# Performance work log

Measured on AMD Instinct MI355X. Metric: run time of the kernel, lower is better.

Reference implementation:

```python
import jax, jax.numpy as jnp
import numpy as np

T = 32          # timesteps
GAIN = 1.0      # input_gain
TAU = 2.0       # LIF membrane time constant
VTH = 1.0       # v_threshold
VRESET = 0.0    # v_reset (hard reset)
ALPHA = 2.0     # ATan surrogate alpha


@jax.custom_vjp
def heaviside_atan(x):
    # forward: Heaviside spike; backward: ATan surrogate gradient
    return (x >= 0).astype(x.dtype)

def _hs_fwd(x):
    return heaviside_atan(x), x

def _hs_bwd(x, g):
    # d/dx ATan surrogate: (alpha/2) / (1 + (pi/2 * alpha * x)^2)
    return (g * (ALPHA / 2.0) / (1.0 + (jnp.pi / 2.0 * ALPHA * x) ** 2),)

heaviside_atan.defvjp(_hs_fwd, _hs_bwd)


def lif_multistep(cur_seq):
    """Multi-step LIF over cur_seq [T, B, H]; hard reset, detach_reset=True."""
    def step(v, x):
        # charge: v = v + (x - (v - v_reset)) / tau
        v = v + (x - (v - VRESET)) / TAU
        spike = heaviside_atan(v - VTH)
        sd = jax.lax.stop_gradient(spike)  # detach_reset
        v = (1.0 - sd) * v + sd * VRESET   # hard reset
        return v, spike

    v0 = jnp.full(cur_seq.shape[1:], VRESET, dtype=cur_seq.dtype)
    _, spikes = jax.lax.scan(step, v0, cur_seq)
    return spikes


def setup_inputs() -> dict:
    key = jax.random.key(0)
    ks = jax.random.split(key, 4)

    def xavier(k, o, i):
        lim = np.sqrt(6.0 / (i + o)).astype(np.float32)
        return jax.random.uniform(k, (o, i), minval=-lim, maxval=lim, dtype=jnp.float32)

    x_flat = jax.random.uniform(ks[0], (512, 784), dtype=jnp.float32)
    W0 = xavier(ks[1], 1024, 784)
    b0 = jnp.zeros((1024,), jnp.float32)
    W1 = xavier(ks[2], 1024, 1024)
    b1 = jnp.zeros((1024,), jnp.float32)
    W2 = xavier(ks[3], 10, 1024)
    b2 = jnp.zeros((10,), jnp.float32)
    return {"x_flat": x_flat, "W0": W0, "b0": b0, "W1": W1, "b1": b1, "W2": W2, "b2": b2}


def reference(x_flat, W0, b0, W1, b1, W2, b2):
    # repeat_static_input: [B, 784] -> [T, B, 784]
    h = jnp.broadcast_to(x_flat * GAIN, (T,) + x_flat.shape)
    count = None
    for W, b in ((W0, b0), (W1, b1), (W2, b2)):
        cur = jnp.einsum('tbi,oi->tbo', h, W) + b  # fc over all timesteps
        spk = lif_multistep(cur)                   # [T, B, out]
        count = spk.sum(axis=0)                    # spike counts [B, out]
        h = spk
    # predict() returns argmax(count); return the final count (logits) here
    return count
```

## Files before the change

kernel.cpp:

```cpp
#include <hip/hip_runtime.h>
#include <hip/hip_bf16.h>
#include <stdint.h>


typedef __bf16 bf16x8 __attribute__((ext_vector_type(8)));
typedef float  f32x4  __attribute__((ext_vector_type(4)));

__device__ __forceinline__ void gload16(const void* g, void* l) {
  __builtin_amdgcn_global_load_lds((const __attribute__((address_space(1))) void*)g,
                                   (__attribute__((address_space(3))) void*)l,
                                   16, 0, 0);
}

__device__ __forceinline__ void bsplit3(float v, __hip_bfloat16& h,
                                        __hip_bfloat16& m, __hip_bfloat16& l) {
  h = __float2bfloat16(v);
  float r1 = v - __bfloat162float(h);
  m = __float2bfloat16(r1);
  float r2 = r1 - __bfloat162float(m);
  l = __float2bfloat16(r2);
}

__global__ __launch_bounds__(256) void prep_k(const float* __restrict__ x,
                                              const float* __restrict__ W0,
                                              __hip_bfloat16* __restrict__ Ax,
                                              __hip_bfloat16* __restrict__ Bw) {
  const int bid = blockIdx.x, tid = threadIdx.x;
  if (bid < 1600) {
    int i = bid * 256 + tid;
    int m = i / 800, k = i - m * 800;
    float v = (k < 784) ? x[(size_t)m * 784 + k] : 0.f;
    __hip_bfloat16 h, mm, l;
    bsplit3(v, h, mm, l);
    size_t base = (size_t)m * 4800;
    Ax[base + k] = h;         Ax[base + 800 + k] = h;
    Ax[base + 1600 + k] = mm; Ax[base + 2400 + k] = mm;
    Ax[base + 3200 + k] = h;  Ax[base + 4000 + k] = l;
  } else {
    int i = (bid - 1600) * 256 + tid;
    int n = i / 800, k = i - n * 800;
    float v = (k < 784) ? W0[(size_t)n * 784 + k] : 0.f;
    __hip_bfloat16 h, mm, l;
    bsplit3(v, h, mm, l);
    size_t base = (size_t)n * 4800;
    Bw[base + k] = h;         Bw[base + 800 + k] = mm;
    Bw[base + 1600 + k] = h;  Bw[base + 2400 + k] = mm;
    Bw[base + 3200 + k] = l;  Bw[base + 4000 + k] = h;
  }
}

__global__ __launch_bounds__(256, 2) void gemm0t_k(const __hip_bfloat16* __restrict__ A,
                                                   const __hip_bfloat16* __restrict__ B,
                                                   const float* __restrict__ W1,
                                                   float* __restrict__ W1T,
                                                   float* __restrict__ Cpart) {
  __shared__ __align__(16) char smem[16384];
  const int bid = blockIdx.x, tid = threadIdx.x;

  if (bid >= 320) {
    float (*t)[33] = (float(*)[33])smem;
    int tt = bid - 320;
    int c0 = (tt & 31) * 32, r0 = (tt >> 5) * 32;
    int lx = tid & 31, ly = tid >> 5;
#pragma unroll
    for (int i = 0; i < 32; i += 8)
      t[ly + i][lx] = W1[(size_t)(r0 + ly + i) * 1024 + (c0 + lx)];
    __syncthreads();
#pragma unroll
    for (int i = 0; i < 32; i += 8)
      W1T[(size_t)(c0 + ly + i) * 1024 + (r0 + lx)] = t[lx][ly + i];
    return;
  }

  __hip_bfloat16* As = (__hip_bfloat16*)smem;
  __hip_bfloat16* Bs = As + 128 * 32;
  const int bx = bid & 3, by = (bid >> 2) & 7, bz = bid >> 5;
  const int wave = tid >> 6, lane = tid & 63, quad = lane >> 4, l16 = lane & 15;
  const int wm = (wave >> 1) * 64, wn = (wave & 1) * 64;
  const int mbase = bx * 128, nbase = by * 128, kbase = bz * 480;
  const int srow = lane >> 2;
  const int gq = (lane & 3) ^ ((lane >> 3) & 3);
  const int swz = (l16 >> 1) & 3;
  f32x4 acc[4][4] = {};
  for (int kk = kbase; kk < kbase + 480; kk += 32) {
#pragma unroll
    for (int r = 0; r < 2; ++r) {
      int grp = wave * 2 + r;
      gload16(A + (size_t)(mbase + grp * 16 + srow) * 4800 + kk + gq * 8,
              (char*)As + grp * 1024);
      gload16(B + (size_t)(nbase + grp * 16 + srow) * 4800 + kk + gq * 8,
              (char*)Bs + grp * 1024);
    }
    __syncthreads();
    const __bf16* Ab = (const __bf16*)As;
    const __bf16* Bb = (const __bf16*)Bs;
    bf16x8 af[4], bfr[4];
#pragma unroll
    for (int i = 0; i < 4; ++i)
      af[i] = *(const bf16x8*)(Ab + (wm + i * 16 + l16) * 32 + ((quad ^ swz) * 8));
#pragma unroll
    for (int j = 0; j < 4; ++j)
      bfr[j] = *(const bf16x8*)(Bb + (wn + j * 16 + l16) * 32 + ((quad ^ swz) * 8));
#pragma unroll
    for (int i = 0; i < 4; ++i)
#pragma unroll
      for (int j = 0; j < 4; ++j)
        acc[i][j] = __builtin_amdgcn_mfma_f32_16x16x32_bf16(af[i], bfr[j], acc[i][j], 0, 0, 0);
    __syncthreads();
  }
  float* Cz = Cpart + (size_t)bz * 512 * 1024;
#pragma unroll
  for (int i = 0; i < 4; ++i)
#pragma unroll
    for (int j = 0; j < 4; ++j)
#pragma unroll
      for (int r = 0; r < 4; ++r) {
        int m = mbase + wm + i * 16 + quad * 4 + r;
        int n = nbase + wn + j * 16 + l16;
        Cz[(size_t)m * 1024 + n] = acc[i][j][r];
      }
}

struct TailSM {
  unsigned short sidx[1024];
  int sseg[33];
  int mtot;
  unsigned l2i[1024];
  unsigned l2w[1024];
  union {
    struct { int whist[16][33]; int clstot[33]; int clsofs[34]; int wofs[16][33]; } s3;
    struct { int wtot[16]; int wbase[16]; } s4;
    struct { float sW2[10 * 1025]; float scur[320]; } s5;
  } u;
};

__global__ __launch_bounds__(1024) void tail_k(const float* __restrict__ Cpart,
                                               const float* __restrict__ b0,
                                               const float* __restrict__ W1T,
                                               const float* __restrict__ b1,
                                               const float* __restrict__ W2,
                                               const float* __restrict__ b2,
                                               float* __restrict__ out) {
  __shared__ TailSM sm;
  const int b = blockIdx.x, o = threadIdx.x;
  const int wave = o >> 6, lane = o & 63;

  {
    float cur = 0.f;
#pragma unroll
    for (int z = 0; z < 10; ++z)
      cur += Cpart[(size_t)z * 512 * 1024 + (size_t)b * 1024 + o];
    cur += b0[o];
    float v = 0.f;
    unsigned word = 0u;
#pragma unroll
    for (int t = 0; t < 32; ++t) {
      v = v + (cur - v) * 0.5f;
      if (v >= 1.0f) { word |= 1u << t; v = 0.f; }
    }
    int n = word ? (__builtin_ctz(word) + 1) : 0;
    unsigned long long mymask = 0ull;
#pragma unroll 1
    for (int c = 1; c <= 32; ++c) {
      unsigned long long m = __ballot(n == c);
      if (lane == 0) sm.u.s3.whist[wave][c] = __popcll(m);
      if (n == c) mymask = m;
    }
    __syncthreads();
    if (o < 32) {
      int c = o + 1, s = 0;
#pragma unroll
      for (int w = 0; w < 16; ++w) s += sm.u.s3.whist[w][c];
      sm.u.s3.clstot[c] = s;
    }
    __syncthreads();
    if (o == 0) {
      int run = 0;
#pragma unroll
      for (int c = 1; c <= 32; ++c) { sm.u.s3.clsofs[c] = run; run += sm.u.s3.clstot[c]; }
      sm.u.s3.clsofs[33] = run;
    }
    __syncthreads();
    if (o < 32) {
      int c = o + 1, s = sm.u.s3.clsofs[c];
#pragma unroll
      for (int w = 0; w < 16; ++w) { sm.u.s3.wofs[w][c] = s; s += sm.u.s3.whist[w][c]; }
    }
    __syncthreads();
    if (n) {
      int pos = sm.u.s3.wofs[wave][n] + __popcll(mymask & ((1ull << lane) - 1ull));
      sm.sidx[pos] = (unsigned short)o;
    }
    if (o < 33) sm.sseg[o] = sm.u.s3.clsofs[o + 1];
  }
  __syncthreads();

  {
    float S[32];
#pragma unroll
    for (int c = 0; c < 32; ++c) {
      int j0 = __builtin_amdgcn_readfirstlane((c == 0) ? 0 : sm.sseg[c - 1]);
      int j1 = __builtin_amdgcn_readfirstlane(sm.sseg[c]);
      float s = 0.f;
      for (int j = j0; j < j1; ++j)
        s += W1T[(size_t)sm.sidx[j] * 1024 + o];
      S[c] = s;
    }
    const float bias = b1[o];
    float v = 0.f;
    unsigned word = 0u;
#pragma unroll
    for (int t = 0; t < 32; ++t) {
      float cur = 0.f;
#pragma unroll
      for (int c = 1; c <= 32; ++c)
        if ((t + 1) % c == 0) cur += S[c - 1];
      float xc = cur + bias;
      v = v + (xc - v) * 0.5f;
      if (v >= 1.0f) { word |= 1u << t; v = 0.f; }
    }
    bool act = (word != 0u);
    unsigned long long m = __ballot(act);
    if (lane == 0) sm.u.s4.wtot[wave] = __popcll(m);
    __syncthreads();
    if (o == 0) {
      int s = 0;
#pragma unroll
      for (int i = 0; i < 16; ++i) { sm.u.s4.wbase[i] = s; s += sm.u.s4.wtot[i]; }
      sm.mtot = s;
    }
    __syncthreads();
    if (act) {
      int pos = sm.u.s4.wbase[wave] + __popcll(m & ((1ull << lane) - 1ull));
      sm.l2i[pos] = (unsigned)o;
      sm.l2w[pos] = word;
    }
  }
  __syncthreads();

  {
    for (int i = o; i < 10240; i += 1024)
      sm.u.s5.sW2[(i >> 10) * 1025 + (i & 1023)] = W2[i];
    __syncthreads();
    const int mtot = sm.mtot;
    if (o < 320) {
      int t = o / 10, c = o - t * 10;
      float acc = 0.f;
      for (int j = 0; j < mtot; ++j) {
        unsigned wd = sm.l2w[j];
        float wv = sm.u.s5.sW2[c * 1025 + sm.l2i[j]];
        acc += ((wd >> t) & 1u) ? wv : 0.f;
      }
      sm.u.s5.scur[o] = acc;
    }
    __syncthreads();
    if (o < 10) {
      float v = 0.f, cnt2 = 0.f, bias = b2[o];
#pragma unroll
      for (int tt = 0; tt < 32; ++tt) {
        float xc = sm.u.s5.scur[tt * 10 + o] + bias;
        v = v + (xc - v) * 0.5f;
        if (v >= 1.0f) { cnt2 += 1.f; v = 0.f; }
      }
      out[(size_t)b * 10 + o] = cnt2;
    }
  }
}

extern "C" void kernel_launch(void* const* d_in, const int* in_sizes, int n_in,
                              void* d_out, int out_size, void* d_ws, size_t ws_size,
                              hipStream_t stream) {
  const float* x  = (const float*)d_in[0];
  const float* W0 = (const float*)d_in[1];
  const float* b0 = (const float*)d_in[2];
  const float* W1 = (const float*)d_in[3];
  const float* b1 = (const float*)d_in[4];
  const float* W2 = (const float*)d_in[5];
  const float* b2 = (const float*)d_in[6];
  float* out = (float*)d_out;

  char* ws = (char*)d_ws;
  size_t off = 0;
  auto alloc = [&](size_t bytes) -> char* {
    char* p = ws + off;
    off += (bytes + 255) & ~(size_t)255;
    return p;
  };
  __hip_bfloat16* Ax    = (__hip_bfloat16*)alloc((size_t)512 * 4800 * 2);
  __hip_bfloat16* Bw    = (__hip_bfloat16*)alloc((size_t)1024 * 4800 * 2);
  float*          Cpart = (float*)alloc((size_t)10 * 512 * 1024 * 4);
  float*          W1T   = (float*)alloc((size_t)1024 * 1024 * 4);
  (void)ws_size;

  prep_k<<<4800, 256, 0, stream>>>(x, W0, Ax, Bw);
  gemm0t_k<<<1344, 256, 0, stream>>>(Ax, Bw, W1, W1T, Cpart);
  tail_k<<<512, 1024, 0, stream>>>(Cpart, b0, W1T, b1, W2, b2, out);
}
```

Measured before the change: 110.4 us.

## Store compact bf16 split planes and remap GEMM K segments to them

The prep kernel now writes only three bf16 planes (hi, mid, lo) per row instead of six duplicated ones, and uses vectorized 4-wide float loads and 4-wide bf16 stores. The GEMM computes which plane each 800-wide K segment maps to for A and B, so the split-bf16 product stays the same. This is meant to halve the prep writes and the workspace footprint, and to raise L2 reuse in the GEMM. The change also raises wave priority around the MFMA block with s_setprio.

```diff
diff --git a/kernel.cpp b/kernel.cpp
--- a/kernel.cpp
+++ b/kernel.cpp
@@ -5,6 +5,7 @@
 
 typedef __bf16 bf16x8 __attribute__((ext_vector_type(8)));
 typedef float  f32x4  __attribute__((ext_vector_type(4)));
+typedef unsigned short u16x4 __attribute__((ext_vector_type(4)));
 
 __device__ __forceinline__ void gload16(const void* g, void* l) {
   __builtin_amdgcn_global_load_lds((const __attribute__((address_space(1))) void*)g,
@@ -26,27 +27,31 @@
                                               __hip_bfloat16* __restrict__ Ax,
                                               __hip_bfloat16* __restrict__ Bw) {
   const int bid = blockIdx.x, tid = threadIdx.x;
-  if (bid < 1600) {
-    int i = bid * 256 + tid;
-    int m = i / 800, k = i - m * 800;
-    float v = (k < 784) ? x[(size_t)m * 784 + k] : 0.f;
-    __hip_bfloat16 h, mm, l;
-    bsplit3(v, h, mm, l);
-    size_t base = (size_t)m * 4800;
-    Ax[base + k] = h;         Ax[base + 800 + k] = h;
-    Ax[base + 1600 + k] = mm; Ax[base + 2400 + k] = mm;
-    Ax[base + 3200 + k] = h;  Ax[base + 4000 + k] = l;
-  } else {
-    int i = (bid - 1600) * 256 + tid;
-    int n = i / 800, k = i - n * 800;
-    float v = (k < 784) ? W0[(size_t)n * 784 + k] : 0.f;
-    __hip_bfloat16 h, mm, l;
-    bsplit3(v, h, mm, l);
-    size_t base = (size_t)n * 4800;
-    Bw[base + k] = h;         Bw[base + 800 + k] = mm;
-    Bw[base + 1600 + k] = h;  Bw[base + 2400 + k] = mm;
-    Bw[base + 3200 + k] = l;  Bw[base + 4000 + k] = h;
-  }
+  const float* src;
+  __hip_bfloat16* dst;
+  int i;
+  if (bid < 400) { i = bid * 256 + tid; src = x;  dst = Ax; }
+  else           { i = (bid - 400) * 256 + tid; src = W0; dst = Bw; }
+  const int row = i / 200;
+  const int k0 = (i - row * 200) * 4;
+
+  f32x4 v = {0.f, 0.f, 0.f, 0.f};
+  if (k0 < 784)
+    v = *(const f32x4*)(src + (size_t)row * 784 + k0);
+
+  u16x4 hv, mv, lv;
+#pragma unroll
+  for (int e = 0; e < 4; ++e) {
+    __hip_bfloat16 h, m, l;
+    bsplit3(v[e], h, m, l);
+    hv[e] = __builtin_bit_cast(unsigned short, h);
+    mv[e] = __builtin_bit_cast(unsigned short, m);
+    lv[e] = __builtin_bit_cast(unsigned short, l);
+  }
+  __hip_bfloat16* p = dst + (size_t)row * 2400 + k0;
+  *(u16x4*)(p)        = hv;
+  *(u16x4*)(p + 800)  = mv;
+  *(u16x4*)(p + 1600) = lv;
 }
 
 __global__ __launch_bounds__(256, 2) void gemm0t_k(const __hip_bfloat16* __restrict__ A,
@@ -83,12 +88,18 @@
   const int swz = (l16 >> 1) & 3;
   f32x4 acc[4][4] = {};
   for (int kk = kbase; kk < kbase + 480; kk += 32) {
+    const int seg = kk / 800;
+    const int rem = kk - seg * 800;
+    const int abase = (seg == 2 || seg == 3) ? 800 : (seg == 5 ? 1600 : 0);
+    const int bbase = (seg == 1 || seg == 3) ? 800 : (seg == 4 ? 1600 : 0);
+    const __hip_bfloat16* Ak = A + abase + rem;
+    const __hip_bfloat16* Bk = B + bbase + rem;
 #pragma unroll
     for (int r = 0; r < 2; ++r) {
       int grp = wave * 2 + r;
-      gload16(A + (size_t)(mbase + grp * 16 + srow) * 4800 + kk + gq * 8,
+      gload16(Ak + (size_t)(mbase + grp * 16 + srow) * 2400 + gq * 8,
               (char*)As + grp * 1024);
-      gload16(B + (size_t)(nbase + grp * 16 + srow) * 4800 + kk + gq * 8,
+      gload16(Bk + (size_t)(nbase + grp * 16 + srow) * 2400 + gq * 8,
               (char*)Bs + grp * 1024);
     }
     __syncthreads();
@@ -101,11 +112,13 @@
 #pragma unroll
     for (int j = 0; j < 4; ++j)
       bfr[j] = *(const bf16x8*)(Bb + (wn + j * 16 + l16) * 32 + ((quad ^ swz) * 8));
+    __builtin_amdgcn_s_setprio(1);
 #pragma unroll
     for (int i = 0; i < 4; ++i)
 #pragma unroll
       for (int j = 0; j < 4; ++j)
         acc[i][j] = __builtin_amdgcn_mfma_f32_16x16x32_bf16(af[i], bfr[j], acc[i][j], 0, 0, 0);
+    __builtin_amdgcn_s_setprio(0);
     __syncthreads();
   }
   float* Cz = Cpart + (size_t)bz * 512 * 1024;
@@ -286,13 +299,13 @@
     off += (bytes + 255) & ~(size_t)255;
     return p;
   };
-  __hip_bfloat16* Ax    = (__hip_bfloat16*)alloc((size_t)512 * 4800 * 2);
-  __hip_bfloat16* Bw    = (__hip_bfloat16*)alloc((size_t)1024 * 4800 * 2);
+  __hip_bfloat16* Ax    = (__hip_bfloat16*)alloc((size_t)512 * 2400 * 2);
+  __hip_bfloat16* Bw    = (__hip_bfloat16*)alloc((size_t)1024 * 2400 * 2);
   float*          Cpart = (float*)alloc((size_t)10 * 512 * 1024 * 4);
   float*          W1T   = (float*)alloc((size_t)1024 * 1024 * 4);
   (void)ws_size;
 
-  prep_k<<<4800, 256, 0, stream>>>(x, W0, Ax, Bw);
+  prep_k<<<1200, 256, 0, stream>>>(x, W0, Ax, Bw);
   gemm0t_k<<<1344, 256, 0, stream>>>(Ax, Bw, W1, W1T, Cpart);
   tail_k<<<512, 1024, 0, stream>>>(Cpart, b0, W1T, b1, W2, b2, out);
 }
```

Result: no change. 110.7 us (+0.3%).
